# Kernel tuning notes

Measured on AMD Instinct MI355X. Metric: run time of the kernel, lower is better.

Reference implementation:

```python
import jax, jax.numpy as jnp
import numpy as np

B, N, D, E = 8, 10000, 64, 160000


def setup_inputs() -> dict:
    key = jax.random.key(0)
    ks = jax.random.split(key, 7)
    x = jax.random.normal(ks[0], (B, N, D), dtype=jnp.float32)
    W0 = jax.random.normal(ks[1], (D, D), dtype=jnp.float32) / np.sqrt(D)
    W1 = jax.random.normal(ks[2], (D, D), dtype=jnp.float32) / np.sqrt(D)
    W2 = jax.random.normal(ks[3], (D, D), dtype=jnp.float32) / np.sqrt(D)
    adj_vals = jax.random.uniform(ks[4], (E,), dtype=jnp.float32)
    adj_rows = jax.random.randint(ks[5], (E,), 0, N, dtype=jnp.int32)
    adj_cols = jax.random.randint(ks[6], (E,), 0, N, dtype=jnp.int32)
    return {"x": x, "W0": W0, "W1": W1, "W2": W2,
            "adj_vals": adj_vals, "adj_rows": adj_rows, "adj_cols": adj_cols}


def _spmm(vals, rows, cols, h):
    # h: [B, N, D]; shared sparse adj in COO. out[b, r] += vals[e] * h[b, c]
    msg = h[:, cols, :] * vals[None, :, None]          # [B, E, D]
    return jnp.zeros_like(h).at[:, rows, :].add(msg)   # scatter-add over rows


def _layer(h, W, vals, rows, cols):
    h = jax.nn.relu(jnp.einsum('bnd,df->bnf', h, W))   # Linear (no bias) + act
    return _spmm(vals, rows, cols, h)                  # adj @ h per sample


def reference(x, W0, W1, W2, adj_vals, adj_rows, adj_cols):
    out = _layer(x, W0.T, adj_vals, adj_rows, adj_cols)
    out = _layer(out, W1.T, adj_vals, adj_rows, adj_cols)
    out = _layer(out, W2.T, adj_vals, adj_rows, adj_cols)
    return out
```

## Files before the change

### kernel.cpp

```cpp
#include <hip/hip_runtime.h>
#include <hip/hip_bf16.h>


#define GCN_B 8
#define GCN_N 10000
#define GCN_D 64
#define GCN_E 160000
#define GCN_BN (GCN_B * GCN_N)
#define GCN_CAP 64

typedef __attribute__((ext_vector_type(8))) short short8v;
typedef __attribute__((ext_vector_type(4))) float float4v;

static __device__ __forceinline__ unsigned short f2bf(float f) {
    __hip_bfloat16 h = __float2bfloat16(f);
    return *reinterpret_cast<unsigned short*>(&h);
}

__global__ __launch_bounds__(256) void zero_cvt_kernel(
    int* __restrict__ cur,
    const float* __restrict__ W0, const float* __restrict__ W1,
    const float* __restrict__ W2, unsigned short* __restrict__ Wb)
{
    int i = blockIdx.x * 256 + threadIdx.x;
    if (i < GCN_N) cur[i] = 0;
    if (i < 4096)        Wb[i] = f2bf(W0[i]);
    else if (i < 8192)   Wb[i] = f2bf(W1[i - 4096]);
    else if (i < 12288)  Wb[i] = f2bf(W2[i - 8192]);
}

__global__ __launch_bounds__(256) void scatter_gemm1_kernel(
    const float* __restrict__ vals, const int* __restrict__ rows,
    const int* __restrict__ cols, int* __restrict__ cur,
    float* __restrict__ pval, int* __restrict__ pcol,
    const float* __restrict__ hin,
    const unsigned short* __restrict__ Wb,
    unsigned char* __restrict__ t8,
    float* __restrict__ sc)
{
    __shared__ unsigned short hs[64 * 72];
    __shared__ unsigned short wsm[64 * 72];

    const int tid = threadIdx.x;

    if (blockIdx.x < 625) {
        int e = blockIdx.x * 256 + tid;
        if (e < GCN_E) {
            int r = rows[e];
            int pos = atomicAdd(&cur[r], 1);
            if (pos < GCN_CAP) {
                pval[(size_t)r * GCN_CAP + pos] = vals[e];
                pcol[(size_t)r * GCN_CAP + pos] = cols[e];
            }
        }
        return;
    }

    const int g0 = (blockIdx.x - 625) * 64;

    {
        const int row = tid >> 2, seg = tid & 3;
        const uint4* src = reinterpret_cast<const uint4*>(Wb + row * 64 + seg * 16);
        uint4 a = src[0], b = src[1];
        *reinterpret_cast<uint4*>(&wsm[row * 72 + seg * 16])     = a;
        *reinterpret_cast<uint4*>(&wsm[row * 72 + seg * 16 + 8]) = b;
    }
    {
        const int row = tid >> 2, seg = tid & 3;
        const int g = g0 + row;
        const int n = g >> 3, b = g & 7;
        const float4* src = reinterpret_cast<const float4*>(
            hin + ((size_t)b * GCN_N + n) * 64 + seg * 16);
        float4 v0 = src[0], v1 = src[1], v2 = src[2], v3 = src[3];
        float vv[16] = {v0.x, v0.y, v0.z, v0.w, v1.x, v1.y, v1.z, v1.w,
                        v2.x, v2.y, v2.z, v2.w, v3.x, v3.y, v3.z, v3.w};
        unsigned int p[8];
#pragma unroll
        for (int j = 0; j < 8; ++j)
            p[j] = (unsigned int)f2bf(vv[2 * j]) |
                   ((unsigned int)f2bf(vv[2 * j + 1]) << 16);
        *reinterpret_cast<uint4*>(&hs[row * 72 + seg * 16]) =
            make_uint4(p[0], p[1], p[2], p[3]);
        *reinterpret_cast<uint4*>(&hs[row * 72 + seg * 16 + 8]) =
            make_uint4(p[4], p[5], p[6], p[7]);
    }
    __syncthreads();

    const int w = tid >> 6;
    const int l = tid & 63;
    const int rbase = w * 16;
    const int arow = rbase + (l & 15);
    const int koff = (l >> 4) * 8;

    float4v acc[4];
#pragma unroll
    for (int nt = 0; nt < 4; ++nt) acc[nt] = (float4v){0.f, 0.f, 0.f, 0.f};

#pragma unroll
    for (int kc = 0; kc < 2; ++kc) {
        short8v afrag = *reinterpret_cast<const short8v*>(
            &hs[arow * 72 + kc * 32 + koff]);
#pragma unroll
        for (int nt = 0; nt < 4; ++nt) {
            short8v bfrag = *reinterpret_cast<const short8v*>(
                &wsm[(nt * 16 + (l & 15)) * 72 + kc * 32 + koff]);
            acc[nt] = __builtin_amdgcn_mfma_f32_16x16x32_bf16(
                afrag, bfrag, acc[nt], 0, 0, 0);
        }
    }

    const int crow = rbase + (l >> 4) * 4;
    const int col = l & 15;
#pragma unroll
    for (int r4 = 0; r4 < 4; ++r4) {
        float v0 = fmaxf(acc[0][r4], 0.0f);
        float v1 = fmaxf(acc[1][r4], 0.0f);
        float v2 = fmaxf(acc[2][r4], 0.0f);
        float v3 = fmaxf(acc[3][r4], 0.0f);
        float m = fmaxf(fmaxf(v0, v1), fmaxf(v2, v3));
        m = fmaxf(m, __shfl_xor(m, 1, 64));
        m = fmaxf(m, __shfl_xor(m, 2, 64));
        m = fmaxf(m, __shfl_xor(m, 4, 64));
        m = fmaxf(m, __shfl_xor(m, 8, 64));
        const float inv = (m > 0.0f) ? 255.0f / m : 0.0f;
        const size_t g = (size_t)(g0 + crow + r4);
        t8[g * 64 +  0 + col] = (unsigned char)rintf(v0 * inv);
        t8[g * 64 + 16 + col] = (unsigned char)rintf(v1 * inv);
        t8[g * 64 + 32 + col] = (unsigned char)rintf(v2 * inv);
        t8[g * 64 + 48 + col] = (unsigned char)rintf(v3 * inv);
        if (col == 0) sc[g] = m * (1.0f / 255.0f);
    }
}

static __device__ __forceinline__ void gather_row_i8(
    const uint2* __restrict__ t8, const float* __restrict__ sc,
    const float* __restrict__ pval, const int* __restrict__ pcol,
    int r, int deg, int lane, float* a)
{
    const int beg = r * GCN_CAP;
    const int bidx = lane >> 3;
#pragma unroll 8
    for (int j = beg; j < beg + deg; ++j) {
        const float v = pval[j];
        const int c = pcol[j];
        const float s = v * sc[c * 8 + bidx];
        uint2 u = t8[(size_t)c * 64 + lane];
        a[0] += s * (float)( u.x        & 0xff);
        a[1] += s * (float)((u.x >>  8) & 0xff);
        a[2] += s * (float)((u.x >> 16) & 0xff);
        a[3] += s * (float)( u.x >> 24);
        a[4] += s * (float)( u.y        & 0xff);
        a[5] += s * (float)((u.y >>  8) & 0xff);
        a[6] += s * (float)((u.y >> 16) & 0xff);
        a[7] += s * (float)( u.y >> 24);
    }
}

__global__ __launch_bounds__(512) void spmm_gemm_fused(
    const uint2* __restrict__ t8_in,
    const float* __restrict__ sc_in,
    const float* __restrict__ pval,
    const int* __restrict__ pcol,
    const int* __restrict__ deg,
    const unsigned short* __restrict__ Wb,
    unsigned char* __restrict__ t8_out,
    float* __restrict__ sc_out)
{
    __shared__ unsigned short hs[64 * 72];
    __shared__ unsigned short wsm[64 * 72];

    const int tid = threadIdx.x;
    const int g0 = blockIdx.x * 64;

    {
        const int row = tid >> 3, seg = tid & 7;
        uint4 v = *reinterpret_cast<const uint4*>(Wb + row * 64 + seg * 8);
        *reinterpret_cast<uint4*>(&wsm[row * 72 + seg * 8]) = v;
    }

    const int w = tid >> 6;
    const int lane = tid & 63;
    const int r = blockIdx.x * 8 + w;
    int d = deg[r]; if (d > GCN_CAP) d = GCN_CAP;

    float a[8];
#pragma unroll
    for (int i = 0; i < 8; ++i) a[i] = 0.f;
    gather_row_i8(t8_in, sc_in, pval, pcol, r, d, lane, a);

    {
        unsigned int p[4];
#pragma unroll
        for (int k = 0; k < 4; ++k)
            p[k] = (unsigned int)f2bf(a[2 * k]) |
                   ((unsigned int)f2bf(a[2 * k + 1]) << 16);
        *reinterpret_cast<uint4*>(
            &hs[(w * 8 + (lane >> 3)) * 72 + (lane & 7) * 8]) =
            make_uint4(p[0], p[1], p[2], p[3]);
    }
    __syncthreads();

    const int q = w >> 1, pr = w & 1;
    const int arow = q * 16 + (lane & 15);
    const int koff = (lane >> 4) * 8;

    float4v acc[2];
    acc[0] = (float4v){0.f, 0.f, 0.f, 0.f};
    acc[1] = (float4v){0.f, 0.f, 0.f, 0.f};

#pragma unroll
    for (int kc = 0; kc < 2; ++kc) {
        short8v afrag = *reinterpret_cast<const short8v*>(
            &hs[arow * 72 + kc * 32 + koff]);
#pragma unroll
        for (int nt2 = 0; nt2 < 2; ++nt2) {
            const int nt = pr * 2 + nt2;
            short8v bfrag = *reinterpret_cast<const short8v*>(
                &wsm[(nt * 16 + (lane & 15)) * 72 + kc * 32 + koff]);
            acc[nt2] = __builtin_amdgcn_mfma_f32_16x16x32_bf16(
                afrag, bfrag, acc[nt2], 0, 0, 0);
        }
    }

    const int crow = q * 16 + (lane >> 4) * 4;
    const int col = lane & 15;
    float v[2][4];
#pragma unroll
    for (int nt2 = 0; nt2 < 2; ++nt2)
#pragma unroll
        for (int r4 = 0; r4 < 4; ++r4)
            v[nt2][r4] = fmaxf(acc[nt2][r4], 0.0f);

    __syncthreads();
    float* pm = reinterpret_cast<float*>(hs);
    float* scl = reinterpret_cast<float*>(wsm);
#pragma unroll
    for (int r4 = 0; r4 < 4; ++r4)
        pm[(crow + r4) * 32 + pr * 16 + col] = fmaxf(v[0][r4], v[1][r4]);
    __syncthreads();

    if (tid < 64) {
        float m = 0.f;
        const float* p = &pm[tid * 32];
#pragma unroll 8
        for (int j = 0; j < 32; ++j) m = fmaxf(m, p[j]);
        scl[tid] = m;
        sc_out[g0 + tid] = m * (1.0f / 255.0f);
    }
    __syncthreads();

#pragma unroll
    for (int r4 = 0; r4 < 4; ++r4) {
        const float m = scl[crow + r4];
        const float inv = (m > 0.0f) ? 255.0f / m : 0.0f;
        const size_t g = (size_t)(g0 + crow + r4);
#pragma unroll
        for (int nt2 = 0; nt2 < 2; ++nt2) {
            const int nt = pr * 2 + nt2;
            t8_out[g * 64 + nt * 16 + col] =
                (unsigned char)rintf(v[nt2][r4] * inv);
        }
    }
}

__global__ __launch_bounds__(256) void spmm_final(
    const uint2* __restrict__ t8,
    const float* __restrict__ sc,
    const float* __restrict__ pval,
    const int* __restrict__ pcol,
    const int* __restrict__ deg,
    float* __restrict__ outf)
{
    const int r = (blockIdx.x * 256 + threadIdx.x) >> 6;
    const int lane = threadIdx.x & 63;
    if (r >= GCN_N) return;
    int d = deg[r]; if (d > GCN_CAP) d = GCN_CAP;

    float a[8];
#pragma unroll
    for (int i = 0; i < 8; ++i) a[i] = 0.f;
    gather_row_i8(t8, sc, pval, pcol, r, d, lane, a);

    const int b = lane >> 3;
    const int d0 = (lane & 7) * 8;
    float* op = outf + ((size_t)b * GCN_N + r) * 64 + d0;
    *reinterpret_cast<float4*>(op)     = make_float4(a[0], a[1], a[2], a[3]);
    *reinterpret_cast<float4*>(op + 4) = make_float4(a[4], a[5], a[6], a[7]);
}

extern "C" void kernel_launch(void* const* d_in, const int* in_sizes, int n_in,
                              void* d_out, int out_size, void* d_ws, size_t ws_size,
                              hipStream_t stream) {
    const float* x    = (const float*)d_in[0];
    const float* W0   = (const float*)d_in[1];
    const float* W1   = (const float*)d_in[2];
    const float* W2   = (const float*)d_in[3];
    const float* vals = (const float*)d_in[4];
    const int*   rows = (const int*)d_in[5];
    const int*   cols = (const int*)d_in[6];

    const size_t t8_bytes = (size_t)GCN_BN * GCN_D;
    const size_t sc_bytes = (size_t)GCN_BN * 4;

    char* ws = (char*)d_ws;
    unsigned char* tA8 = (unsigned char*)ws;
    size_t off = (t8_bytes + 255) / 256 * 256;
    float* scA  = (float*)(ws + off); off += (sc_bytes + 255) / 256 * 256;
    float* sc2  = (float*)(ws + off); off += (sc_bytes + 255) / 256 * 256;
    int*   cur  = (int*)(ws + off); off += (GCN_N * 4 + 255) / 256 * 256;
    float* pval = (float*)(ws + off); off += (size_t)GCN_N * GCN_CAP * 4;
    int*   pcol = (int*)(ws + off); off += (size_t)GCN_N * GCN_CAP * 4;
    unsigned short* Wb = (unsigned short*)(ws + off); off += 3 * 4096 * 2;

    unsigned char* t28 = (unsigned char*)d_out;
    float* outf = (float*)d_out;

    const int gemm_grid = GCN_BN / 64;
    const int edge_grid = (GCN_E + 255) / 256;
    const int spmm_grid = (GCN_N * 64 + 255) / 256;

    zero_cvt_kernel<<<48, 256, 0, stream>>>(cur, W0, W1, W2, Wb);
    scatter_gemm1_kernel<<<edge_grid + gemm_grid, 256, 0, stream>>>(
        vals, rows, cols, cur, pval, pcol, x, Wb, tA8, scA);

    spmm_gemm_fused<<<gemm_grid, 512, 0, stream>>>(
        (const uint2*)tA8, scA, pval, pcol, cur, Wb + 4096, t28, sc2);
    spmm_gemm_fused<<<gemm_grid, 512, 0, stream>>>(
        (const uint2*)t28, sc2, pval, pcol, cur, Wb + 8192, tA8, scA);
    spmm_final<<<spmm_grid, 256, 0, stream>>>(
        (const uint2*)tA8, scA, pval, pcol, cur, outf);
}
```

Baseline: 95.34 us.

## Pack bf16 edge value and column into one word; process more rows per block

The per-row edge lists go from separate float value and int column arrays to one 32-bit word per edge: the bf16 value in the high half and the column index in the low half. This halves the metadata read per edge in every gather. The fused SpMM+GEMM kernel now handles 16 graph rows (128 GEMM rows) per block, and the final SpMM does 4 rows per wave, which cuts block count and amortises the weight staging. In exchange, edge weights lose precision to bf16, and column indices must fit in 16 bits (N=10000 fits).

```diff
diff --git a/kernel.cpp b/kernel.cpp
--- a/kernel.cpp
+++ b/kernel.cpp
@@ -32,7 +32,7 @@
 __global__ __launch_bounds__(256) void scatter_gemm1_kernel(
     const float* __restrict__ vals, const int* __restrict__ rows,
     const int* __restrict__ cols, int* __restrict__ cur,
-    float* __restrict__ pval, int* __restrict__ pcol,
+    unsigned int* __restrict__ pedge,
     const float* __restrict__ hin,
     const unsigned short* __restrict__ Wb,
     unsigned char* __restrict__ t8,
@@ -49,8 +49,9 @@
             int r = rows[e];
             int pos = atomicAdd(&cur[r], 1);
             if (pos < GCN_CAP) {
-                pval[(size_t)r * GCN_CAP + pos] = vals[e];
-                pcol[(size_t)r * GCN_CAP + pos] = cols[e];
+                unsigned int word = ((unsigned int)f2bf(vals[e]) << 16) |
+                                    (unsigned int)cols[e];
+                pedge[(size_t)r * GCN_CAP + pos] = word;
             }
         }
         return;
@@ -134,15 +135,16 @@
 
 static __device__ __forceinline__ void gather_row_i8(
     const uint2* __restrict__ t8, const float* __restrict__ sc,
-    const float* __restrict__ pval, const int* __restrict__ pcol,
+    const unsigned int* __restrict__ pedge,
     int r, int deg, int lane, float* a)
 {
     const int beg = r * GCN_CAP;
     const int bidx = lane >> 3;
 #pragma unroll 8
     for (int j = beg; j < beg + deg; ++j) {
-        const float v = pval[j];
-        const int c = pcol[j];
+        const unsigned int ew = pedge[j];
+        const int c = ew & 0xffff;
+        const float v = __uint_as_float(ew & 0xffff0000u);
         const float s = v * sc[c * 8 + bidx];
         uint2 u = t8[(size_t)c * 64 + lane];
         a[0] += s * (float)( u.x        & 0xff);
@@ -159,18 +161,18 @@
 __global__ __launch_bounds__(512) void spmm_gemm_fused(
     const uint2* __restrict__ t8_in,
     const float* __restrict__ sc_in,
-    const float* __restrict__ pval,
-    const int* __restrict__ pcol,
+    const unsigned int* __restrict__ pedge,
     const int* __restrict__ deg,
     const unsigned short* __restrict__ Wb,
     unsigned char* __restrict__ t8_out,
     float* __restrict__ sc_out)
 {
-    __shared__ unsigned short hs[64 * 72];
+    __shared__ unsigned short hs[128 * 72];
     __shared__ unsigned short wsm[64 * 72];
 
     const int tid = threadIdx.x;
-    const int g0 = blockIdx.x * 64;
+    const int r0 = blockIdx.x * 16;
+    const int G0 = r0 * 8;
 
     {
         const int row = tid >> 3, seg = tid & 7;
@@ -180,112 +182,131 @@
 
     const int w = tid >> 6;
     const int lane = tid & 63;
-    const int r = blockIdx.x * 8 + w;
-    int d = deg[r]; if (d > GCN_CAP) d = GCN_CAP;
-
-    float a[8];
-#pragma unroll
-    for (int i = 0; i < 8; ++i) a[i] = 0.f;
-    gather_row_i8(t8_in, sc_in, pval, pcol, r, d, lane, a);
-
-    {
+
+#pragma unroll
+    for (int half = 0; half < 2; ++half) {
+        const int r = r0 + half * 8 + w;
+        int d = deg[r]; if (d > GCN_CAP) d = GCN_CAP;
+        float a[8];
+#pragma unroll
+        for (int i = 0; i < 8; ++i) a[i] = 0.f;
+        gather_row_i8(t8_in, sc_in, pedge, r, d, lane, a);
+
         unsigned int p[4];
 #pragma unroll
         for (int k = 0; k < 4; ++k)
             p[k] = (unsigned int)f2bf(a[2 * k]) |
                    ((unsigned int)f2bf(a[2 * k + 1]) << 16);
         *reinterpret_cast<uint4*>(
-            &hs[(w * 8 + (lane >> 3)) * 72 + (lane & 7) * 8]) =
+            &hs[(half * 64 + w * 8 + (lane >> 3)) * 72 + (lane & 7) * 8]) =
             make_uint4(p[0], p[1], p[2], p[3]);
     }
     __syncthreads();
 
     const int q = w >> 1, pr = w & 1;
-    const int arow = q * 16 + (lane & 15);
     const int koff = (lane >> 4) * 8;
 
-    float4v acc[2];
-    acc[0] = (float4v){0.f, 0.f, 0.f, 0.f};
-    acc[1] = (float4v){0.f, 0.f, 0.f, 0.f};
-
-#pragma unroll
-    for (int kc = 0; kc < 2; ++kc) {
-        short8v afrag = *reinterpret_cast<const short8v*>(
-            &hs[arow * 72 + kc * 32 + koff]);
-#pragma unroll
-        for (int nt2 = 0; nt2 < 2; ++nt2) {
-            const int nt = pr * 2 + nt2;
-            short8v bfrag = *reinterpret_cast<const short8v*>(
-                &wsm[(nt * 16 + (lane & 15)) * 72 + kc * 32 + koff]);
-            acc[nt2] = __builtin_amdgcn_mfma_f32_16x16x32_bf16(
-                afrag, bfrag, acc[nt2], 0, 0, 0);
+    float4v acc[2][2];
+#pragma unroll
+    for (int half = 0; half < 2; ++half)
+#pragma unroll
+        for (int nt2 = 0; nt2 < 2; ++nt2)
+            acc[half][nt2] = (float4v){0.f, 0.f, 0.f, 0.f};
+
+#pragma unroll
+    for (int half = 0; half < 2; ++half) {
+        const int arow = half * 64 + q * 16 + (lane & 15);
+#pragma unroll
+        for (int kc = 0; kc < 2; ++kc) {
+            short8v afrag = *reinterpret_cast<const short8v*>(
+                &hs[arow * 72 + kc * 32 + koff]);
+#pragma unroll
+            for (int nt2 = 0; nt2 < 2; ++nt2) {
+                const int nt = pr * 2 + nt2;
+                short8v bfrag = *reinterpret_cast<const short8v*>(
+                    &wsm[(nt * 16 + (lane & 15)) * 72 + kc * 32 + koff]);
+                acc[half][nt2] = __builtin_amdgcn_mfma_f32_16x16x32_bf16(
+                    afrag, bfrag, acc[half][nt2], 0, 0, 0);
+            }
         }
     }
 
     const int crow = q * 16 + (lane >> 4) * 4;
     const int col = lane & 15;
-    float v[2][4];
-#pragma unroll
-    for (int nt2 = 0; nt2 < 2; ++nt2)
-#pragma unroll
-        for (int r4 = 0; r4 < 4; ++r4)
-            v[nt2][r4] = fmaxf(acc[nt2][r4], 0.0f);
+    float v[2][2][4];
+#pragma unroll
+    for (int half = 0; half < 2; ++half)
+#pragma unroll
+        for (int nt2 = 0; nt2 < 2; ++nt2)
+#pragma unroll
+            for (int r4 = 0; r4 < 4; ++r4)
+                v[half][nt2][r4] = fmaxf(acc[half][nt2][r4], 0.0f);
 
     __syncthreads();
     float* pm = reinterpret_cast<float*>(hs);
     float* scl = reinterpret_cast<float*>(wsm);
 #pragma unroll
-    for (int r4 = 0; r4 < 4; ++r4)
-        pm[(crow + r4) * 32 + pr * 16 + col] = fmaxf(v[0][r4], v[1][r4]);
-    __syncthreads();
-
-    if (tid < 64) {
+    for (int half = 0; half < 2; ++half)
+#pragma unroll
+        for (int r4 = 0; r4 < 4; ++r4)
+            pm[(half * 64 + crow + r4) * 32 + pr * 16 + col] =
+                fmaxf(v[half][0][r4], v[half][1][r4]);
+    __syncthreads();
+
+    if (tid < 128) {
         float m = 0.f;
         const float* p = &pm[tid * 32];
 #pragma unroll 8
         for (int j = 0; j < 32; ++j) m = fmaxf(m, p[j]);
         scl[tid] = m;
-        sc_out[g0 + tid] = m * (1.0f / 255.0f);
-    }
-    __syncthreads();
-
-#pragma unroll
-    for (int r4 = 0; r4 < 4; ++r4) {
-        const float m = scl[crow + r4];
-        const float inv = (m > 0.0f) ? 255.0f / m : 0.0f;
-        const size_t g = (size_t)(g0 + crow + r4);
-#pragma unroll
-        for (int nt2 = 0; nt2 < 2; ++nt2) {
-            const int nt = pr * 2 + nt2;
-            t8_out[g * 64 + nt * 16 + col] =
-                (unsigned char)rintf(v[nt2][r4] * inv);
+        sc_out[G0 + tid] = m * (1.0f / 255.0f);
+    }
+    __syncthreads();
+
+#pragma unroll
+    for (int half = 0; half < 2; ++half)
+#pragma unroll
+        for (int r4 = 0; r4 < 4; ++r4) {
+            const int lrow = half * 64 + crow + r4;
+            const float m = scl[lrow];
+            const float inv = (m > 0.0f) ? 255.0f / m : 0.0f;
+            const size_t g = (size_t)(G0 + lrow);
+#pragma unroll
+            for (int nt2 = 0; nt2 < 2; ++nt2) {
+                const int nt = pr * 2 + nt2;
+                t8_out[g * 64 + nt * 16 + col] =
+                    (unsigned char)rintf(v[half][nt2][r4] * inv);
+            }
         }
-    }
 }
 
 __global__ __launch_bounds__(256) void spmm_final(
     const uint2* __restrict__ t8,
     const float* __restrict__ sc,
-    const float* __restrict__ pval,
-    const int* __restrict__ pcol,
+    const unsigned int* __restrict__ pedge,
     const int* __restrict__ deg,
     float* __restrict__ outf)
 {
-    const int r = (blockIdx.x * 256 + threadIdx.x) >> 6;
+    const int w = threadIdx.x >> 6;
     const int lane = threadIdx.x & 63;
-    if (r >= GCN_N) return;
-    int d = deg[r]; if (d > GCN_CAP) d = GCN_CAP;
-
-    float a[8];
-#pragma unroll
-    for (int i = 0; i < 8; ++i) a[i] = 0.f;
-    gather_row_i8(t8, sc, pval, pcol, r, d, lane, a);
-
-    const int b = lane >> 3;
-    const int d0 = (lane & 7) * 8;
-    float* op = outf + ((size_t)b * GCN_N + r) * 64 + d0;
-    *reinterpret_cast<float4*>(op)     = make_float4(a[0], a[1], a[2], a[3]);
-    *reinterpret_cast<float4*>(op + 4) = make_float4(a[4], a[5], a[6], a[7]);
+    const int r0 = blockIdx.x * 16 + w * 4;
+
+#pragma unroll
+    for (int k = 0; k < 4; ++k) {
+        const int r = r0 + k;
+        int d = deg[r]; if (d > GCN_CAP) d = GCN_CAP;
+
+        float a[8];
+#pragma unroll
+        for (int i = 0; i < 8; ++i) a[i] = 0.f;
+        gather_row_i8(t8, sc, pedge, r, d, lane, a);
+
+        const int b = lane >> 3;
+        const int d0 = (lane & 7) * 8;
+        float* op = outf + ((size_t)b * GCN_N + r) * 64 + d0;
+        *reinterpret_cast<float4*>(op)     = make_float4(a[0], a[1], a[2], a[3]);
+        *reinterpret_cast<float4*>(op + 4) = make_float4(a[4], a[5], a[6], a[7]);
+    }
 }
 
 extern "C" void kernel_launch(void* const* d_in, const int* in_sizes, int n_in,
@@ -308,8 +329,8 @@
     float* scA  = (float*)(ws + off); off += (sc_bytes + 255) / 256 * 256;
     float* sc2  = (float*)(ws + off); off += (sc_bytes + 255) / 256 * 256;
     int*   cur  = (int*)(ws + off); off += (GCN_N * 4 + 255) / 256 * 256;
-    float* pval = (float*)(ws + off); off += (size_t)GCN_N * GCN_CAP * 4;
-    int*   pcol = (int*)(ws + off); off += (size_t)GCN_N * GCN_CAP * 4;
+    unsigned int* pedge = (unsigned int*)(ws + off);
+    off += (size_t)GCN_N * GCN_CAP * 4;
     unsigned short* Wb = (unsigned short*)(ws + off); off += 3 * 4096 * 2;
 
     unsigned char* t28 = (unsigned char*)d_out;
@@ -317,16 +338,17 @@
 
     const int gemm_grid = GCN_BN / 64;
     const int edge_grid = (GCN_E + 255) / 256;
-    const int spmm_grid = (GCN_N * 64 + 255) / 256;
+    const int fuse_grid = GCN_N / 16;
+    const int finl_grid = GCN_N / 16;
 
     zero_cvt_kernel<<<48, 256, 0, stream>>>(cur, W0, W1, W2, Wb);
     scatter_gemm1_kernel<<<edge_grid + gemm_grid, 256, 0, stream>>>(
-        vals, rows, cols, cur, pval, pcol, x, Wb, tA8, scA);
-
-    spmm_gemm_fused<<<gemm_grid, 512, 0, stream>>>(
-        (const uint2*)tA8, scA, pval, pcol, cur, Wb + 4096, t28, sc2);
-    spmm_gemm_fused<<<gemm_grid, 512, 0, stream>>>(
-        (const uint2*)t28, sc2, pval, pcol, cur, Wb + 8192, tA8, scA);
-    spmm_final<<<spmm_grid, 256, 0, stream>>>(
-        (const uint2*)tA8, scA, pval, pcol, cur, outf);
-}
+        vals, rows, cols, cur, pedge, x, Wb, tA8, scA);
+
+    spmm_gemm_fused<<<fuse_grid, 512, 0, stream>>>(
+        (const uint2*)tA8, scA, pedge, cur, Wb + 4096, t28, sc2);
+    spmm_gemm_fused<<<fuse_grid, 512, 0, stream>>>(
+        (const uint2*)t28, sc2, pedge, cur, Wb + 8192, tA8, scA);
+    spmm_final<<<finl_grid, 256, 0, stream>>>(
+        (const uint2*)tA8, scA, pedge, cur, outf);
+}
```

After: 118.6 us. 1.24x slower.
